# Kernel tuning notes

Measured on AMD Instinct MI355X. Metric: run time of the kernel, lower is better.

Reference implementation:

```python
import jax, jax.numpy as jnp
import numpy as np

LAYERS = [2048, 2048, 2048, 512]
THRESHOLD = 1.0
TAU_MEM = 20.0
TAU_SYN = 5.0
DT = 1.0
BATCH = 32
T = 100


def setup_inputs() -> dict:
    key = jax.random.key(0)
    ks = jax.random.split(key, 2 + 2 * (len(LAYERS) - 1))
    inp = {
        "x": jax.random.uniform(ks[0], (BATCH, LAYERS[0]), dtype=jnp.float32),
        "noise": jax.random.uniform(ks[1], (T, BATCH, LAYERS[0]), dtype=jnp.float32),
        "time_steps": T,
    }
    # nn.Linear-style init: U(-1/sqrt(fan_in), 1/sqrt(fan_in))
    for i in range(len(LAYERS) - 1):
        fan_in, fan_out = LAYERS[i], LAYERS[i + 1]
        bound = 1.0 / np.sqrt(fan_in)
        inp[f"W{i}"] = jax.random.uniform(ks[2 + 2 * i], (fan_out, fan_in), minval=-bound, maxval=bound, dtype=jnp.float32)
        inp[f"b{i}"] = jax.random.uniform(ks[3 + 2 * i], (fan_out,), minval=-bound, maxval=bound, dtype=jnp.float32)
    return inp


def _lif_step(I, mem, syn):
    # dI_syn/dt = -I_syn/tau_syn + I ; dV/dt = -V/tau_mem + I_syn  (explicit Euler, dt=1)
    syn = syn + (-syn / TAU_SYN + I) * DT
    mem = mem + (-mem / TAU_MEM + syn) * DT
    spikes = (mem >= THRESHOLD).astype(mem.dtype)
    mem = mem * (1.0 - spikes)          # reset fired neurons
    mem = mem * (mem > 0).astype(mem.dtype)  # clamp negative potentials to 0
    return spikes, mem, syn


def reference(x, noise, W0, b0, W1, b1, W2, b2, time_steps):
    params = [(W0, b0), (W1, b1), (W2, b2)]
    batch = x.shape[0]
    dtype = x.dtype
    rate = jnp.clip(x, 0.0, 1.0)                       # [B, in]
    in_spikes = (noise < rate[None]).astype(dtype)     # [T, B, in] Poisson encoding

    mems = tuple(jnp.zeros((batch, W.shape[0]), dtype) for W, _ in params)
    syns = tuple(jnp.zeros((batch, W.shape[0]), dtype) for W, _ in params)

    def step(carry, sp_in):
        mems, syns = carry
        layer_in = sp_in
        new_mems, new_syns = [], []
        count = jnp.zeros((), dtype)
        for (W, b), m, s in zip(params, mems, syns):
            I = layer_in @ W.T + b
            spk, m, s = _lif_step(I, m, s)
            new_mems.append(m)
            new_syns.append(s)
            count = count + spk.sum()
            layer_in = spk
        return (tuple(new_mems), tuple(new_syns)), (layer_in, count)

    (_, _), (out_spikes, counts) = jax.lax.scan(step, (mems, syns), in_spikes)
    output = out_spikes.mean(axis=0)   # [B, out]: time-averaged output spike train
    total_spikes = counts.sum()
    return output, total_spikes
```

## Files before the change

kernel.cpp:

```cpp
#include <hip/hip_runtime.h>

#define T_STEPS 100
#define MTOT    3200
#define R0_OFF  0
#define R1_OFF  13107200
#define I_OFF   26214400

typedef _Float16 half8_t __attribute__((ext_vector_type(8)));
typedef _Float16 half4_t __attribute__((ext_vector_type(4)));
typedef float    f32x4   __attribute__((ext_vector_type(4)));

__device__ __forceinline__ void encode_body(
    int blk, const float* __restrict__ x, const float* __restrict__ noise,
    _Float16* __restrict__ spk0, float* __restrict__ out)
{
    if (blk == 0 && threadIdx.x == 0) out[16384] = 0.0f;
    const int tid = threadIdx.x;
    const int m0  = blk * 16;
    __shared__ half8_t lds[16 * 257];
    #pragma unroll
    for (int ml = 0; ml < 16; ++ml) {
        const int m = m0 + ml;
        const int t = m >> 5, b = m & 31;
        const float4 x1 = *(const float4*)(x + b * 2048 + tid * 8);
        const float4 x2 = *(const float4*)(x + b * 2048 + tid * 8 + 4);
        const float4 n1 = *(const float4*)(noise + (size_t)t * 65536 + b * 2048 + tid * 8);
        const float4 n2 = *(const float4*)(noise + (size_t)t * 65536 + b * 2048 + tid * 8 + 4);
        const float xr[8] = {x1.x,x1.y,x1.z,x1.w,x2.x,x2.y,x2.z,x2.w};
        const float nz[8] = {n1.x,n1.y,n1.z,n1.w,n2.x,n2.y,n2.z,n2.w};
        half8_t sp;
        #pragma unroll
        for (int j = 0; j < 8; ++j) {
            const float r = fminf(fmaxf(xr[j], 0.0f), 1.0f);
            sp[j] = (nz[j] < r) ? (_Float16)1.0f : (_Float16)0.0f;
        }
        lds[ml * 257 + tid] = sp;
    }
    __syncthreads();
    #pragma unroll
    for (int r = 0; r < 16; ++r) {
        const int ml  = tid & 15;
        const int oct = r * 16 + (tid >> 4);
        *(half8_t*)(spk0 + ((size_t)oct * MTOT + m0 + ml) * 8) = lds[ml * 257 + oct];
    }
}

__device__ __forceinline__ void convw_body(
    int blk, const float* __restrict__ W, _Float16* __restrict__ Wf)
{
    const int koct = threadIdx.x;
    #pragma unroll
    for (int r = 0; r < 8; ++r) {
        const int row = blk * 8 + r;
        const float* wp = W + (size_t)row * 2048 + koct * 8;
        const float4 f1 = *(const float4*)(wp);
        const float4 f2 = *(const float4*)(wp + 4);
        half8_t h = {(_Float16)f1.x,(_Float16)f1.y,(_Float16)f1.z,(_Float16)f1.w,
                     (_Float16)f2.x,(_Float16)f2.y,(_Float16)f2.z,(_Float16)f2.w};
        const size_t idx = (size_t)(row >> 4) * 32768
                         + ((size_t)((koct >> 2) * 64 + (koct & 3) * 16 + (row & 15))) * 8;
        *(half8_t*)(Wf + idx) = h;
    }
}

__device__ __forceinline__ void scan_body(
    int blk, const _Float16* __restrict__ I, const float* __restrict__ bias,
    _Float16* __restrict__ spk_out, float* __restrict__ out,
    const int nshift, const int is_last)
{
    const int gid = blk * 256 + threadIdx.x;
    const int N = 1 << nshift;
    const int n = gid & (N - 1);
    const int b = gid >> nshift;
    const float bi = bias[n];
    const size_t nbase = (size_t)(n >> 3) * (MTOT * 8) + (n & 7);
    float mem = 0.f, syn = 0.f, osum = 0.f, cnt = 0.f;
    #pragma unroll 4
    for (int t = 0; t < T_STEPS; ++t) {
        const int m = t * 32 + b;
        const float Iv = (float)I[nbase + (size_t)m * 8] + bi;
        syn = syn + (-syn / 5.0f + Iv);
        mem = mem + (-mem / 20.0f + syn);
        const float sv = (mem >= 1.0f) ? 1.0f : 0.0f;
        mem = (sv != 0.0f) ? 0.0f : mem;
        mem = (mem > 0.0f) ? mem : 0.0f;
        cnt += sv; osum += sv;
        if (!is_last) spk_out[nbase + (size_t)m * 8] = (_Float16)sv;
    }
    if (is_last) out[b * 512 + n] = osum * 0.01f;
    float c = cnt;
    #pragma unroll
    for (int s2 = 1; s2 < 64; s2 <<= 1) c += __shfl_xor(c, s2);
    if ((threadIdx.x & 63) == 0) atomicAdd(&out[16384], c);
}

__global__ __launch_bounds__(256, 2) void snn_enc_convw_kernel(
    const float* __restrict__ x, const float* __restrict__ noise,
    _Float16* __restrict__ spk0, float* __restrict__ out,
    const float* __restrict__ W, _Float16* __restrict__ Wf)
{
    if (blockIdx.x < 200) encode_body(blockIdx.x, x, noise, spk0, out);
    else                  convw_body(blockIdx.x - 200, W, Wf);
}

__global__ __launch_bounds__(256, 4) void snn_scan_convw_kernel(
    const _Float16* __restrict__ I, const float* __restrict__ bias,
    _Float16* __restrict__ spk_out, float* __restrict__ out,
    const int scan_blocks, const int nshift,
    const float* __restrict__ W, _Float16* __restrict__ Wf)
{
    if ((int)blockIdx.x < scan_blocks)
        scan_body(blockIdx.x, I, bias, spk_out, out, nshift, 0);
    else
        convw_body(blockIdx.x - scan_blocks, W, Wf);
}

__global__ __launch_bounds__(256, 4) void snn_scan_kernel(
    const _Float16* __restrict__ I, const float* __restrict__ bias,
    float* __restrict__ out, const int nshift)
{
    scan_body(blockIdx.x, I, bias, nullptr, out, nshift, 1);
}


__device__ __forceinline__ half8_t ldB(const _Float16* __restrict__ p, int kq) {
    return *(const half8_t*)(p + (size_t)kq * (MTOT * 8));
}

template<bool HAS2, int KB>
__device__ __forceinline__ void gemm64_half(
    const _Float16* __restrict__ wlds,
    const _Float16* const (&bp)[2],
    half8_t (&bE)[2], half8_t (&bO)[2],
    f32x4 (&acc)[2][4],
    const int lane, const int quad)
{
    #pragma unroll 2
    for (int kbl = 0; kbl < 32; kbl += 2) {
        half8_t a[4];
        #pragma unroll
        for (int s = 0; s < 4; ++s)
            a[s] = *(const half8_t*)(wlds + (size_t)s * 16384 + (size_t)(kbl * 64 + lane) * 8);
        #pragma unroll
        for (int s = 0; s < 4; ++s) {
            acc[0][s] = __builtin_amdgcn_mfma_f32_16x16x32_f16(a[s], bE[0], acc[0][s], 0, 0, 0);
            if (HAS2)
                acc[1][s] = __builtin_amdgcn_mfma_f32_16x16x32_f16(a[s], bE[1], acc[1][s], 0, 0, 0);
        }
        if (KB + kbl + 2 < 64) {
            const int kq = (KB + kbl + 2) * 4 + quad;
            bE[0] = ldB(bp[0], kq);
            if (HAS2) bE[1] = ldB(bp[1], kq);
        }
        half8_t c[4];
        #pragma unroll
        for (int s = 0; s < 4; ++s)
            c[s] = *(const half8_t*)(wlds + (size_t)s * 16384 + (size_t)((kbl + 1) * 64 + lane) * 8);
        #pragma unroll
        for (int s = 0; s < 4; ++s) {
            acc[0][s] = __builtin_amdgcn_mfma_f32_16x16x32_f16(c[s], bO[0], acc[0][s], 0, 0, 0);
            if (HAS2)
                acc[1][s] = __builtin_amdgcn_mfma_f32_16x16x32_f16(c[s], bO[1], acc[1][s], 0, 0, 0);
        }
        if (KB + kbl + 3 < 64) {
            const int kq = (KB + kbl + 3) * 4 + quad;
            bO[0] = ldB(bp[0], kq);
            if (HAS2) bO[1] = ldB(bp[1], kq);
        }
    }
}

template<int NC>
__global__ __launch_bounds__(1024, 4) void snn_gemm64_kernel(
    const _Float16* __restrict__ Wf, const _Float16* __restrict__ spk,
    _Float16* __restrict__ I)
{
    const int tid  = threadIdx.x;
    const int lane = tid & 63;
    const int w    = tid >> 6;
    const int mi   = lane & 15;
    const int quad = lane >> 4;
    const int chunk = blockIdx.x % NC;
    const int nbb   = blockIdx.x / NC;
    const int row_base = nbb * 64;
    const int jcount = (200 - chunk + NC - 1) / NC;
    const int rem    = jcount - 16;
    const bool has2  = (w < rem);
    int jl_start = has2 ? (2 * w) : (w + (rem > 0 ? rem : 0));
    if (jl_start < 0) jl_start = 0;
    const bool active = jl_start < jcount;

    int mt[2]; const _Float16* bp[2];
    #pragma unroll
    for (int u = 0; u < 2; ++u) {
        int jl = jl_start + u;
        if (jl >= jcount) jl = jcount - 1;
        mt[u] = chunk + NC * jl;
        bp[u] = spk + ((size_t)mt[u] * 16 + mi) * 8;
    }

    half8_t bE[2], bO[2];
    if (active) {
        bE[0] = ldB(bp[0], quad);
        bO[0] = ldB(bp[0], 4 + quad);
        if (has2) { bE[1] = ldB(bp[1], quad); bO[1] = ldB(bp[1], 4 + quad); }
    }

    __shared__ _Float16 wlds[65536];
    const half8_t* __restrict__ wsrc = (const half8_t*)Wf;
    {
        half8_t* dst = (half8_t*)wlds;
        #pragma unroll
        for (int r = 0; r < 8; ++r) {
            const int flat = r * 1024 + tid;
            const int s = flat >> 11, off = flat & 2047;
            dst[flat] = wsrc[(size_t)(4 * nbb + s) * 4096 + off];
        }
    }
    __syncthreads();

    f32x4 acc[2][4];
    #pragma unroll
    for (int u = 0; u < 2; ++u) {
        #pragma unroll
        for (int s = 0; s < 4; ++s) acc[u][s] = (f32x4){0,0,0,0};
    }

    if (active) {
        if (has2) gemm64_half<true , 0>(wlds, bp, bE, bO, acc, lane, quad);
        else      gemm64_half<false, 0>(wlds, bp, bE, bO, acc, lane, quad);
    }
    __syncthreads();
    {
        half8_t* dst = (half8_t*)wlds;
        #pragma unroll
        for (int r = 0; r < 8; ++r) {
            const int flat = r * 1024 + tid;
            const int s = flat >> 11, off = flat & 2047;
            dst[flat] = wsrc[(size_t)(4 * nbb + s) * 4096 + 2048 + off];
        }
    }
    __syncthreads();
    if (active) {
        if (has2) gemm64_half<true , 32>(wlds, bp, bE, bO, acc, lane, quad);
        else      gemm64_half<false, 32>(wlds, bp, bE, bO, acc, lane, quad);
    }

    if (active) {
        #pragma unroll
        for (int s = 0; s < 4; ++s) {
            const int n0 = row_base + s * 16 + quad * 4;
            const size_t obase = (size_t)(n0 >> 3) * (MTOT * 8) + (n0 & 7);
            #pragma unroll
            for (int u = 0; u < 2; ++u) {
                if (u == 1 && !has2) continue;
                half4_t h;
                #pragma unroll
                for (int r = 0; r < 4; ++r) h[r] = (_Float16)acc[u][s][r];
                *(half4_t*)(I + obase + (size_t)(mt[u] * 16 + mi) * 8) = h;
            }
        }
    }
}

template<int NC, int TPW>
__global__ __launch_bounds__(1024, 4) void snn_gemm_kernel(
    const _Float16* __restrict__ Wf, const _Float16* __restrict__ spk,
    _Float16* __restrict__ I)
{
    const int tid  = threadIdx.x;
    const int lane = tid & 63;
    const int w    = tid >> 6;
    const int quad = lane >> 4, mi = lane & 15;
    const int chunk = blockIdx.x % NC;
    const int nbb   = blockIdx.x / NC;
    const int row_base = nbb * 32;
    const int jcount = (200 - chunk + NC - 1) / NC;

    __shared__ _Float16 wlds[32 * 2048];
    {
        const half8_t* __restrict__ src = (const half8_t*)(Wf + (size_t)nbb * 65536);
        half8_t* __restrict__ dst = (half8_t*)wlds;
        #pragma unroll
        for (int r = 0; r < 8; ++r) dst[tid + r * 1024] = src[tid + r * 1024];
    }
    __syncthreads();

    for (int jl0 = TPW * w; jl0 < jcount; jl0 += 16 * TPW) {
        int mt[TPW]; bool val[TPW];
        const _Float16* bp[TPW];
        #pragma unroll
        for (int u = 0; u < TPW; ++u) {
            const int jl = jl0 + u;
            val[u] = jl < jcount;
            mt[u]  = chunk + NC * (val[u] ? jl : jl0);
            bp[u]  = spk + ((size_t)mt[u] * 16 + mi) * 8;
        }
        f32x4 acc[TPW][2];
        #pragma unroll
        for (int u = 0; u < TPW; ++u) { acc[u][0] = (f32x4){0,0,0,0}; acc[u][1] = (f32x4){0,0,0,0}; }

        half8_t bc[TPW];
        const size_t k0 = (size_t)quad * (MTOT * 8);
        #pragma unroll
        for (int u = 0; u < TPW; ++u) bc[u] = *(const half8_t*)(bp[u] + k0);

        #pragma unroll 4
        for (int kb = 0; kb < 64; ++kb) {
            half8_t bn[TPW];
            if (kb < 63) {
                const size_t kn = (size_t)((kb + 1) * 4 + quad) * (MTOT * 8);
                #pragma unroll
                for (int u = 0; u < TPW; ++u) bn[u] = *(const half8_t*)(bp[u] + kn);
            }
            const half8_t a0 = *(const half8_t*)(wlds + ((size_t)(kb * 64 + lane)) * 8);
            const half8_t a1 = *(const half8_t*)(wlds + 32768 + ((size_t)(kb * 64 + lane)) * 8);
            #pragma unroll
            for (int u = 0; u < TPW; ++u) {
                acc[u][0] = __builtin_amdgcn_mfma_f32_16x16x32_f16(a0, bc[u], acc[u][0], 0, 0, 0);
                acc[u][1] = __builtin_amdgcn_mfma_f32_16x16x32_f16(a1, bc[u], acc[u][1], 0, 0, 0);
            }
            #pragma unroll
            for (int u = 0; u < TPW; ++u) bc[u] = bn[u];
        }
        #pragma unroll
        for (int s = 0; s < 2; ++s) {
            const int n0 = row_base + s * 16 + quad * 4;
            const size_t obase = (size_t)(n0 >> 3) * (MTOT * 8) + (n0 & 7);
            #pragma unroll
            for (int u = 0; u < TPW; ++u) {
                if (!val[u]) continue;
                half4_t h;
                #pragma unroll
                for (int r = 0; r < 4; ++r) h[r] = (_Float16)acc[u][s][r];
                *(half4_t*)(I + obase + (size_t)(mt[u] * 16 + mi) * 8) = h;
            }
        }
    }
}

extern "C" void kernel_launch(void* const* d_in, const int* in_sizes, int n_in,
                              void* d_out, int out_size, void* d_ws, size_t ws_size,
                              hipStream_t stream) {
    const float* x     = (const float*)d_in[0];
    const float* noise = (const float*)d_in[1];
    const float* W0 = (const float*)d_in[3];
    const float* b0 = (const float*)d_in[4];
    const float* W1 = (const float*)d_in[5];
    const float* b1 = (const float*)d_in[6];
    const float* W2 = (const float*)d_in[7];
    const float* b2 = (const float*)d_in[8];
    float* out = (float*)d_out;

    _Float16* R0 = (_Float16*)((char*)d_ws + R0_OFF);
    _Float16* R1 = (_Float16*)((char*)d_ws + R1_OFF);
    _Float16* Ib = (_Float16*)((char*)d_ws + I_OFF);

    snn_enc_convw_kernel<<<dim3(456), dim3(256), 0, stream>>>(x, noise, R0, out, W0, R1);
    snn_gemm64_kernel<8><<<dim3(256), dim3(1024), 0, stream>>>(R1, R0, Ib);
    snn_scan_convw_kernel<<<dim3(512), dim3(256), 0, stream>>>(Ib, b0, R1, out, 256, 11, W1, R0);
    snn_gemm64_kernel<8><<<dim3(256), dim3(1024), 0, stream>>>(R0, R1, Ib);
    snn_scan_convw_kernel<<<dim3(320), dim3(256), 0, stream>>>(Ib, b1, R0, out, 256, 11, W2, R1);
    snn_gemm_kernel<16, 1><<<dim3(256), dim3(1024), 0, stream>>>(R1, R0, Ib);
    snn_scan_kernel<<<dim3(64), dim3(256), 0, stream>>>(Ib, b2, out, 9);

    (void)in_sizes; (void)n_in; (void)out_size; (void)ws_size;
}
```

Measured before the change: 275.5 us.

## Double-buffer weight staging in 64-row GEMM with async global-to-LDS loads

Replaces the two-phase load-then-compute weight staging in the 64-row GEMM kernel with a four-quarter double-buffered pipeline. Weight tiles are copied with global_load_lds directly into shared memory, and explicit vmcnt waits plus barriers let the next quarter load while MFMAs run on the current one. The B-operand prefetch depth grows from 2 to 4 k-steps. The 'active' guard is dropped, which assumes every wave has work for the NC values used. The hand-counted vmcnt values are fragile if the compiler reorders or adds memory operations.

```diff
diff --git a/kernel.cpp b/kernel.cpp
--- a/kernel.cpp
+++ b/kernel.cpp
@@ -127,45 +127,117 @@
     return *(const half8_t*)(p + (size_t)kq * (MTOT * 8));
 }
 
-template<bool HAS2, int KB>
-__device__ __forceinline__ void gemm64_half(
-    const _Float16* __restrict__ wlds,
-    const _Float16* const (&bp)[2],
-    half8_t (&bE)[2], half8_t (&bO)[2],
-    f32x4 (&acc)[2][4],
-    const int lane, const int quad)
-{
-    #pragma unroll 2
-    for (int kbl = 0; kbl < 32; kbl += 2) {
-        half8_t a[4];
-        #pragma unroll
-        for (int s = 0; s < 4; ++s)
-            a[s] = *(const half8_t*)(wlds + (size_t)s * 16384 + (size_t)(kbl * 64 + lane) * 8);
-        #pragma unroll
-        for (int s = 0; s < 4; ++s) {
-            acc[0][s] = __builtin_amdgcn_mfma_f32_16x16x32_f16(a[s], bE[0], acc[0][s], 0, 0, 0);
-            if (HAS2)
-                acc[1][s] = __builtin_amdgcn_mfma_f32_16x16x32_f16(a[s], bE[1], acc[1][s], 0, 0, 0);
-        }
-        if (KB + kbl + 2 < 64) {
-            const int kq = (KB + kbl + 2) * 4 + quad;
-            bE[0] = ldB(bp[0], kq);
-            if (HAS2) bE[1] = ldB(bp[1], kq);
-        }
-        half8_t c[4];
-        #pragma unroll
-        for (int s = 0; s < 4; ++s)
-            c[s] = *(const half8_t*)(wlds + (size_t)s * 16384 + (size_t)((kbl + 1) * 64 + lane) * 8);
-        #pragma unroll
-        for (int s = 0; s < 4; ++s) {
-            acc[0][s] = __builtin_amdgcn_mfma_f32_16x16x32_f16(c[s], bO[0], acc[0][s], 0, 0, 0);
-            if (HAS2)
-                acc[1][s] = __builtin_amdgcn_mfma_f32_16x16x32_f16(c[s], bO[1], acc[1][s], 0, 0, 0);
-        }
-        if (KB + kbl + 3 < 64) {
-            const int kq = (KB + kbl + 3) * 4 + quad;
-            bO[0] = ldB(bp[0], kq);
-            if (HAS2) bO[1] = ldB(bp[1], kq);
+__device__ __forceinline__ void stage_quarter(
+    const _Float16* __restrict__ Wf, _Float16* __restrict__ buf,
+    const int nbb, const int q, const int w, const int lane)
+{
+    #pragma unroll
+    for (int r = 0; r < 4; ++r) {
+        const _Float16* src = Wf + (size_t)(4 * nbb + r) * 32768
+                            + (size_t)q * 8192 + (size_t)(w * 64 + lane) * 8;
+        _Float16* dst = buf + ((size_t)r * 1024 + (size_t)w * 64) * 8;
+        __builtin_amdgcn_global_load_lds(
+            (const __attribute__((address_space(1))) void*)src,
+            (__attribute__((address_space(3))) void*)dst, 16, 0, 0);
+    }
+}
+
+template<bool HAS2>
+__device__ __forceinline__ void boundary() {
+    if (HAS2) asm volatile("s_waitcnt vmcnt(8) lgkmcnt(0)" ::: "memory");
+    else      asm volatile("s_waitcnt vmcnt(4) lgkmcnt(0)" ::: "memory");
+    __builtin_amdgcn_s_barrier();
+    __builtin_amdgcn_sched_barrier(0);
+}
+
+template<bool HAS2>
+__device__ __forceinline__ void kstep(
+    const _Float16* __restrict__ buf, const _Float16* const (&bp)[2],
+    half8_t (&bb)[2], f32x4 (&acc)[2][4],
+    const int lane, const int quad, const int kb, const int kbl)
+{
+    half8_t a[4];
+    #pragma unroll
+    for (int s = 0; s < 4; ++s)
+        a[s] = *(const half8_t*)(buf + (size_t)s * 8192 + (size_t)(kbl * 64 + lane) * 8);
+    #pragma unroll
+    for (int s = 0; s < 4; ++s) {
+        acc[0][s] = __builtin_amdgcn_mfma_f32_16x16x32_f16(a[s], bb[0], acc[0][s], 0, 0, 0);
+        if (HAS2)
+            acc[1][s] = __builtin_amdgcn_mfma_f32_16x16x32_f16(a[s], bb[1], acc[1][s], 0, 0, 0);
+    }
+    if (kb + 4 < 64) {
+        const int kq = (kb + 4) * 4 + quad;
+        bb[0] = ldB(bp[0], kq);
+        if (HAS2) bb[1] = ldB(bp[1], kq);
+    }
+}
+
+template<bool HAS2, int QB>
+__device__ __forceinline__ void quarter(
+    const _Float16* __restrict__ buf, const _Float16* const (&bp)[2],
+    half8_t (&b0)[2], half8_t (&b1)[2], half8_t (&b2)[2], half8_t (&b3)[2],
+    f32x4 (&acc)[2][4], const int lane, const int quad)
+{
+    #pragma unroll
+    for (int k4 = 0; k4 < 16; k4 += 4) {
+        kstep<HAS2>(buf, bp, b0, acc, lane, quad, QB + k4 + 0, k4 + 0);
+        kstep<HAS2>(buf, bp, b1, acc, lane, quad, QB + k4 + 1, k4 + 1);
+        kstep<HAS2>(buf, bp, b2, acc, lane, quad, QB + k4 + 2, k4 + 2);
+        kstep<HAS2>(buf, bp, b3, acc, lane, quad, QB + k4 + 3, k4 + 3);
+    }
+}
+
+template<bool HAS2>
+__device__ __forceinline__ void gemm64_pipe(
+    const _Float16* __restrict__ Wf, _Float16 (*wlds)[32768],
+    const _Float16* const (&bp)[2], const int (&mt)[2],
+    const int nbb, const int row_base, const int w, const int lane,
+    const int quad, const int mi, _Float16* __restrict__ I)
+{
+    half8_t b0[2], b1[2], b2[2], b3[2];
+    b0[0] = ldB(bp[0], quad);      b1[0] = ldB(bp[0], 4 + quad);
+    b2[0] = ldB(bp[0], 8 + quad);  b3[0] = ldB(bp[0], 12 + quad);
+    if (HAS2) {
+        b0[1] = ldB(bp[1], quad);      b1[1] = ldB(bp[1], 4 + quad);
+        b2[1] = ldB(bp[1], 8 + quad);  b3[1] = ldB(bp[1], 12 + quad);
+    }
+    stage_quarter(Wf, wlds[0], nbb, 0, w, lane);
+    stage_quarter(Wf, wlds[1], nbb, 1, w, lane);
+    asm volatile("s_waitcnt vmcnt(4)" ::: "memory");
+    __builtin_amdgcn_s_barrier();
+    __builtin_amdgcn_sched_barrier(0);
+
+    f32x4 acc[2][4];
+    #pragma unroll
+    for (int u = 0; u < 2; ++u) {
+        #pragma unroll
+        for (int s = 0; s < 4; ++s) acc[u][s] = (f32x4){0, 0, 0, 0};
+    }
+
+    quarter<HAS2, 0>(wlds[0], bp, b0, b1, b2, b3, acc, lane, quad);
+    boundary<HAS2>();
+    stage_quarter(Wf, wlds[0], nbb, 2, w, lane);
+    __builtin_amdgcn_sched_barrier(0);
+    quarter<HAS2, 16>(wlds[1], bp, b0, b1, b2, b3, acc, lane, quad);
+    boundary<HAS2>();
+    stage_quarter(Wf, wlds[1], nbb, 3, w, lane);
+    __builtin_amdgcn_sched_barrier(0);
+    quarter<HAS2, 32>(wlds[0], bp, b0, b1, b2, b3, acc, lane, quad);
+    boundary<HAS2>();
+    quarter<HAS2, 48>(wlds[1], bp, b0, b1, b2, b3, acc, lane, quad);
+
+    #pragma unroll
+    for (int s = 0; s < 4; ++s) {
+        const int n0 = row_base + s * 16 + quad * 4;
+        const size_t obase = (size_t)(n0 >> 3) * (MTOT * 8) + (n0 & 7);
+        #pragma unroll
+        for (int u = 0; u < 2; ++u) {
+            if (u == 1 && !HAS2) continue;
+            half4_t h;
+            #pragma unroll
+            for (int r = 0; r < 4; ++r) h[r] = (_Float16)acc[u][s][r];
+            *(half4_t*)(I + obase + (size_t)(mt[u] * 16 + mi) * 8) = h;
         }
     }
 }
@@ -186,9 +258,7 @@
     const int jcount = (200 - chunk + NC - 1) / NC;
     const int rem    = jcount - 16;
     const bool has2  = (w < rem);
-    int jl_start = has2 ? (2 * w) : (w + (rem > 0 ? rem : 0));
-    if (jl_start < 0) jl_start = 0;
-    const bool active = jl_start < jcount;
+    const int jl_start = has2 ? (2 * w) : (w + rem);
 
     int mt[2]; const _Float16* bp[2];
     #pragma unroll
@@ -199,68 +269,10 @@
         bp[u] = spk + ((size_t)mt[u] * 16 + mi) * 8;
     }
 
-    half8_t bE[2], bO[2];
-    if (active) {
-        bE[0] = ldB(bp[0], quad);
-        bO[0] = ldB(bp[0], 4 + quad);
-        if (has2) { bE[1] = ldB(bp[1], quad); bO[1] = ldB(bp[1], 4 + quad); }
-    }
-
-    __shared__ _Float16 wlds[65536];
-    const half8_t* __restrict__ wsrc = (const half8_t*)Wf;
-    {
-        half8_t* dst = (half8_t*)wlds;
-        #pragma unroll
-        for (int r = 0; r < 8; ++r) {
-            const int flat = r * 1024 + tid;
-            const int s = flat >> 11, off = flat & 2047;
-            dst[flat] = wsrc[(size_t)(4 * nbb + s) * 4096 + off];
-        }
-    }
-    __syncthreads();
-
-    f32x4 acc[2][4];
-    #pragma unroll
-    for (int u = 0; u < 2; ++u) {
-        #pragma unroll
-        for (int s = 0; s < 4; ++s) acc[u][s] = (f32x4){0,0,0,0};
-    }
-
-    if (active) {
-        if (has2) gemm64_half<true , 0>(wlds, bp, bE, bO, acc, lane, quad);
-        else      gemm64_half<false, 0>(wlds, bp, bE, bO, acc, lane, quad);
-    }
-    __syncthreads();
-    {
-        half8_t* dst = (half8_t*)wlds;
-        #pragma unroll
-        for (int r = 0; r < 8; ++r) {
-            const int flat = r * 1024 + tid;
-            const int s = flat >> 11, off = flat & 2047;
-            dst[flat] = wsrc[(size_t)(4 * nbb + s) * 4096 + 2048 + off];
-        }
-    }
-    __syncthreads();
-    if (active) {
-        if (has2) gemm64_half<true , 32>(wlds, bp, bE, bO, acc, lane, quad);
-        else      gemm64_half<false, 32>(wlds, bp, bE, bO, acc, lane, quad);
-    }
-
-    if (active) {
-        #pragma unroll
-        for (int s = 0; s < 4; ++s) {
-            const int n0 = row_base + s * 16 + quad * 4;
-            const size_t obase = (size_t)(n0 >> 3) * (MTOT * 8) + (n0 & 7);
-            #pragma unroll
-            for (int u = 0; u < 2; ++u) {
-                if (u == 1 && !has2) continue;
-                half4_t h;
-                #pragma unroll
-                for (int r = 0; r < 4; ++r) h[r] = (_Float16)acc[u][s][r];
-                *(half4_t*)(I + obase + (size_t)(mt[u] * 16 + mi) * 8) = h;
-            }
-        }
-    }
+    __shared__ _Float16 wlds[2][32768];
+
+    if (has2) gemm64_pipe<true >(Wf, wlds, bp, mt, nbb, row_base, w, lane, quad, mi, I);
+    else      gemm64_pipe<false>(Wf, wlds, bp, mt, nbb, row_base, w, lane, quad, mi, I);
 }
 
 template<int NC, int TPW>
```

After: 287.3 us. 1.04x slower.
